# Kernel optimization log

Hardware: AMD Instinct MI355X
Metric: run time of the kernel (lower is better)

Reference implementation:

```python
import jax, jax.numpy as jnp
import numpy as np
from jax import lax

STEP_SIZE = 0.1
T0, T1 = 0.0, 1.0
NUM_STEPS = int(abs(T1 - T0) / STEP_SIZE)  # 10 leapfrog steps

B = 65536
N_DIM = 128      # q and p each have N_DIM dims; x has 2*N_DIM
HIDDEN = 512


def setup_inputs() -> dict:
    key = jax.random.key(0)
    k_x, k_w1, k_w2 = jax.random.split(key, 3)
    x = jax.random.normal(k_x, (B, 2 * N_DIM), dtype=jnp.float32)
    # potential MLP: Linear(N_DIM, HIDDEN) -> tanh -> Linear(HIDDEN, 1)
    W1 = jax.random.normal(k_w1, (N_DIM, HIDDEN), dtype=jnp.float32) / np.sqrt(N_DIM)
    b1 = jnp.zeros((HIDDEN,), dtype=jnp.float32)
    W2 = jax.random.normal(k_w2, (HIDDEN, 1), dtype=jnp.float32) / np.sqrt(HIDDEN)
    b2 = jnp.zeros((1,), dtype=jnp.float32)
    return {"x": x, "W1": W1, "b1": b1, "W2": W2, "b2": b2}


def reference(x, W1, b1, W2, b2):
    """Symplectic (leapfrog-style) forward integration of the Hamiltonian ODE.

    H(q,p) = 0.5*sum(p^2) + V(q), V(q) = MLP(q) with scalar output.
    Per step (faithful to the torch loop, grads taken jointly at (q,p)):
        dH/dq = dV/dq,  dH/dp = p
        p <- p - dV/dq * dt
        q <- q + p_old * dt
    """
    dt = jnp.float32(STEP_SIZE)
    n = x.shape[-1] // 2
    q0, p0 = x[..., :n], x[..., n:]

    def V_sum(q):  # sum over batch of scalar potential
        h = jnp.tanh(q @ W1 + b1)          # [B, HIDDEN]
        v = (h @ W2)[..., 0] + b2[0]       # [B]
        return v.sum()

    grad_V = jax.grad(V_sum)  # [B, n] -> dV/dq per sample (sum decouples)

    def step(carry, _):
        q, p = carry
        dH_dq = grad_V(q)      # grads at (q, p_old)
        dH_dp = p
        p_new = p - dH_dq * dt
        q_new = q + dH_dp * dt
        return (q_new, p_new), None

    (qf, pf), _ = lax.scan(step, (q0, p0), None, length=NUM_STEPS)
    return jnp.concatenate([qf, pf], axis=-1)
```

## Files before the change

### kernel.cpp

```cpp
#include <hip/hip_runtime.h>
#include <hip/hip_bf16.h>

typedef float f32x4 __attribute__((ext_vector_type(4)));
typedef __bf16 bf16x8 __attribute__((ext_vector_type(8)));
typedef unsigned short u16x4 __attribute__((ext_vector_type(4)));

#if defined(__has_builtin)
#if __has_builtin(__builtin_amdgcn_exp2f)
#define EXP2F(x) __builtin_amdgcn_exp2f(x)
#else
#define EXP2F(x) exp2f(x)
#endif
#if __has_builtin(__builtin_amdgcn_rcpf)
#define RCPF(x) __builtin_amdgcn_rcpf(x)
#else
#define RCPF(x) (1.0f/(x))
#endif
#else
#define EXP2F(x) exp2f(x)
#define RCPF(x) (1.0f/(x))
#endif

#define MFMA16(a,b,c) __builtin_amdgcn_mfma_f32_16x16x32_bf16((a),(b),(c),0,0,0)

__device__ __forceinline__ unsigned short f2bf(float f) {
  return __builtin_bit_cast(unsigned short, (__bf16)f);
}

__global__ __launch_bounds__(256) void hn_prep(const float* __restrict__ W1,
                                               unsigned short* __restrict__ W1T) {
  int t = blockIdx.x * 256 + threadIdx.x;
  int rho = t >> 7, io = t & 127;
  int j = (rho >> 5) * 32 + ((rho >> 2) & 3) * 8 + ((rho >> 4) & 1) * 4 + (rho & 3);
  int i = (io >> 5) * 32 + ((io & 7) >> 2) * 16 + ((io >> 3) & 3) * 4 + (io & 7 & 3);
  W1T[t] = f2bf(W1[i * 512 + j]);
}

__global__ __launch_bounds__(512, 2) void hn_main(
    const float* __restrict__ x, const float* __restrict__ W1,
    const float* __restrict__ b1, const float* __restrict__ W2,
    const unsigned short* __restrict__ W1T, float* __restrict__ out) {
  __shared__ __align__(16) char w1l[131072];
  __shared__ __align__(16) float b1s[512];
  __shared__ __align__(16) float w2s[512];

  const int tid = threadIdx.x;
  const int lane = tid & 63;
  const int w = tid >> 6;
  const int m = lane & 15;
  const int g = lane >> 4;

  for (int it = tid; it < 16384; it += 512) {
    int flat = it << 2;
    int i = flat >> 9;
    f32x4 v = *(const f32x4*)(W1 + flat);
    u16x4 pk;
#pragma unroll
    for (int c = 0; c < 4; ++c) pk[c] = f2bf(v[c]);
    int ba = flat << 1;
    *(u16x4*)(w1l + (ba ^ ((i & 7) << 4))) = pk;
  }
  if (tid < 512) {
    b1s[tid] = b1[tid] * 2.8853900817779268f;
    w2s[tid] = W2[tid];
  }
  __syncthreads();

  const int b0 = blockIdx.x * 256 + w * 32;

  float q[2][4][8], p[2][4][8];
#pragma unroll
  for (int bf = 0; bf < 2; ++bf)
#pragma unroll
    for (int kb = 0; kb < 4; ++kb) {
      const float* r0 = x + (long)(b0 + 16 * bf + m) * 256 + kb * 32 + g * 4;
#pragma unroll
      for (int h = 0; h < 2; ++h) {
        f32x4 qv = *(const f32x4*)(r0 + h * 16);
        f32x4 pv = *(const f32x4*)(r0 + h * 16 + 128);
#pragma unroll
        for (int rr = 0; rr < 4; ++rr) {
          q[bf][kb][4 * h + rr] = qv[rr];
          p[bf][kb][4 * h + rr] = pv[rr];
        }
      }
    }

  const char* aptr = (const char*)W1T + m * 256 + g * 16;
  const int s45 = (m & 3) << 4, s6 = (m & 4) << 4;
  const int ybase = ((m * 1024 + g * 16) ^ s45);

#pragma unroll 1
  for (int step = 0; step < 10; ++step) {
    f32x4 gacc[2][8];
#pragma unroll
    for (int bf = 0; bf < 2; ++bf)
#pragma unroll
      for (int nf = 0; nf < 8; ++nf) gacc[bf][nf] = f32x4{0.f, 0.f, 0.f, 0.f};

#pragma unroll 2
    for (int jblk = 0; jblk < 16; ++jblk) {
      f32x4 z[2][2];
      z[0][0] = f32x4{0.f,0.f,0.f,0.f}; z[0][1] = f32x4{0.f,0.f,0.f,0.f};
      z[1][0] = f32x4{0.f,0.f,0.f,0.f}; z[1][1] = f32x4{0.f,0.f,0.f,0.f};
#pragma unroll
      for (int kb = 0; kb < 4; ++kb) {
        bf16x8 qb0, qb1;
#pragma unroll
        for (int r = 0; r < 8; ++r) {
          qb0[r] = (__bf16)q[0][kb][r];
          qb1[r] = (__bf16)q[1][kb][r];
        }
#pragma unroll
        for (int jf = 0; jf < 2; ++jf) {
          bf16x8 a = *(const bf16x8*)(aptr + jblk * 8192 + jf * 4096 + kb * 64);
          z[jf][0] = MFMA16(a, qb0, z[jf][0]);
          z[jf][1] = MFMA16(a, qb1, z[jf][1]);
        }
      }
      float s8[2][8];
#pragma unroll
      for (int jf = 0; jf < 2; ++jf) {
        f32x4 b1v = *(const f32x4*)(b1s + jblk * 32 + g * 8 + jf * 4);
        f32x4 w2v = *(const f32x4*)(w2s + jblk * 32 + g * 8 + jf * 4);
#pragma unroll
        for (int bf = 0; bf < 2; ++bf)
#pragma unroll
          for (int rr = 0; rr < 4; ++rr) {
            float zz = fmaf(z[jf][bf][rr], 2.8853900817779268f, b1v[rr]);
            float e = EXP2F(zz);
            float u = RCPF(e + 1.f);
            float th = fmaf(-2.f, u, 1.f);
            s8[bf][jf * 4 + rr] = fmaf(-th * th, w2v[rr], w2v[rr]);
          }
      }
      bf16x8 sB0, sB1;
#pragma unroll
      for (int r = 0; r < 8; ++r) {
        sB0[r] = (__bf16)s8[0][r];
        sB1[r] = (__bf16)s8[1][r];
      }
      const int joff = (jblk * 64) ^ s6;
#pragma unroll
      for (int nf = 0; nf < 8; ++nf) {
        bf16x8 af = *(const bf16x8*)(w1l + ybase + nf * 16384 + joff);
        gacc[0][nf] = MFMA16(af, sB0, gacc[0][nf]);
        gacc[1][nf] = MFMA16(af, sB1, gacc[1][nf]);
      }
    }

#pragma unroll
    for (int bf = 0; bf < 2; ++bf)
#pragma unroll
      for (int kb = 0; kb < 4; ++kb)
#pragma unroll
        for (int r = 0; r < 8; ++r)
          q[bf][kb][r] = fmaf(0.1f, p[bf][kb][r], q[bf][kb][r]);

#pragma unroll
    for (int bf = 0; bf < 2; ++bf)
#pragma unroll
      for (int kb = 0; kb < 4; ++kb)
#pragma unroll
        for (int r = 0; r < 8; ++r)
          p[bf][kb][r] = fmaf(-0.1f, gacc[bf][2 * kb + (r >> 2)][r & 3], p[bf][kb][r]);

    __syncthreads();
  }

#pragma unroll
  for (int bf = 0; bf < 2; ++bf)
#pragma unroll
    for (int kb = 0; kb < 4; ++kb) {
      float* o = out + (long)(b0 + 16 * bf + m) * 256 + kb * 32 + g * 4;
#pragma unroll
      for (int h = 0; h < 2; ++h) {
        f32x4 qv, pv;
#pragma unroll
        for (int rr = 0; rr < 4; ++rr) {
          qv[rr] = q[bf][kb][4 * h + rr];
          pv[rr] = p[bf][kb][4 * h + rr];
        }
        *(f32x4*)(o + h * 16) = qv;
        *(f32x4*)(o + h * 16 + 128) = pv;
      }
    }
}

extern "C" void kernel_launch(void* const* d_in, const int* in_sizes, int n_in,
                              void* d_out, int out_size, void* d_ws, size_t ws_size,
                              hipStream_t stream) {
  const float* x  = (const float*)d_in[0];
  const float* W1 = (const float*)d_in[1];
  const float* b1 = (const float*)d_in[2];
  const float* W2 = (const float*)d_in[3];
  float* out = (float*)d_out;
  unsigned short* w1t = (unsigned short*)d_ws;

  hipLaunchKernelGGL(hn_prep, dim3(256), dim3(256), 0, stream, W1, w1t);
  hipLaunchKernelGGL(hn_main, dim3(256), dim3(512), 0, stream,
                     x, W1, b1, W2, w1t, out);
}
```

Measured before the change: 345.0 us.

## Use 1024-thread blocks with 16 rows per wave instead of 32

Each wave now handles one 16-row batch fragment instead of two, and each block has 16 waves of 1024 threads, so a block still covers 256 rows. The per-wave register footprint for q, p and the gradient accumulators is halved, which allows more waves per CU to hide MFMA and LDS latency. In exchange, every A-operand load from W1T and the LDS W1 fragments now feeds only one MFMA instead of two, which doubles load traffic per unit of compute. The 128KB LDS per block still limits residency, so the occupancy gain depends on how many blocks fit on a CU.

```diff
diff --git a/kernel.cpp b/kernel.cpp
--- a/kernel.cpp
+++ b/kernel.cpp
@@ -36,7 +36,7 @@
   W1T[t] = f2bf(W1[i * 512 + j]);
 }
 
-__global__ __launch_bounds__(512, 2) void hn_main(
+__global__ __launch_bounds__(1024, 4) void hn_main(
     const float* __restrict__ x, const float* __restrict__ W1,
     const float* __restrict__ b1, const float* __restrict__ W2,
     const unsigned short* __restrict__ W1T, float* __restrict__ out) {
@@ -50,7 +50,7 @@
   const int m = lane & 15;
   const int g = lane >> 4;
 
-  for (int it = tid; it < 16384; it += 512) {
+  for (int it = tid; it < 16384; it += 1024) {
     int flat = it << 2;
     int i = flat >> 9;
     f32x4 v = *(const f32x4*)(W1 + flat);
@@ -66,25 +66,24 @@
   }
   __syncthreads();
 
-  const int b0 = blockIdx.x * 256 + w * 32;
+  const int b0 = blockIdx.x * 256 + w * 16;
+  const float* xrow = x + (long)(b0 + m) * 256;
 
-  float q[2][4][8], p[2][4][8];
+  float q[4][8], p[4][8];
 #pragma unroll
-  for (int bf = 0; bf < 2; ++bf)
+  for (int kb = 0; kb < 4; ++kb) {
+    const float* r0 = xrow + kb * 32 + g * 4;
 #pragma unroll
-    for (int kb = 0; kb < 4; ++kb) {
-      const float* r0 = x + (long)(b0 + 16 * bf + m) * 256 + kb * 32 + g * 4;
+    for (int h = 0; h < 2; ++h) {
+      f32x4 qv = *(const f32x4*)(r0 + h * 16);
+      f32x4 pv = *(const f32x4*)(r0 + h * 16 + 128);
 #pragma unroll
-      for (int h = 0; h < 2; ++h) {
-        f32x4 qv = *(const f32x4*)(r0 + h * 16);
-        f32x4 pv = *(const f32x4*)(r0 + h * 16 + 128);
-#pragma unroll
-        for (int rr = 0; rr < 4; ++rr) {
-          q[bf][kb][4 * h + rr] = qv[rr];
-          p[bf][kb][4 * h + rr] = pv[rr];
-        }
+      for (int rr = 0; rr < 4; ++rr) {
+        q[kb][4 * h + rr] = qv[rr];
+        p[kb][4 * h + rr] = pv[rr];
       }
     }
+  }
 
   const char* aptr = (const char*)W1T + m * 256 + g * 16;
   const int s45 = (m & 3) << 4, s6 = (m & 4) << 4;
@@ -92,99 +91,79 @@
 
 #pragma unroll 1
   for (int step = 0; step < 10; ++step) {
-    f32x4 gacc[2][8];
+    f32x4 gacc[8];
 #pragma unroll
-    for (int bf = 0; bf < 2; ++bf)
-#pragma unroll
-      for (int nf = 0; nf < 8; ++nf) gacc[bf][nf] = f32x4{0.f, 0.f, 0.f, 0.f};
+    for (int nf = 0; nf < 8; ++nf) gacc[nf] = f32x4{0.f, 0.f, 0.f, 0.f};
 
 #pragma unroll 2
     for (int jblk = 0; jblk < 16; ++jblk) {
-      f32x4 z[2][2];
-      z[0][0] = f32x4{0.f,0.f,0.f,0.f}; z[0][1] = f32x4{0.f,0.f,0.f,0.f};
-      z[1][0] = f32x4{0.f,0.f,0.f,0.f}; z[1][1] = f32x4{0.f,0.f,0.f,0.f};
+      f32x4 z[2];
+      z[0] = f32x4{0.f, 0.f, 0.f, 0.f};
+      z[1] = f32x4{0.f, 0.f, 0.f, 0.f};
 #pragma unroll
       for (int kb = 0; kb < 4; ++kb) {
-        bf16x8 qb0, qb1;
+        bf16x8 qb;
 #pragma unroll
-        for (int r = 0; r < 8; ++r) {
-          qb0[r] = (__bf16)q[0][kb][r];
-          qb1[r] = (__bf16)q[1][kb][r];
-        }
+        for (int r = 0; r < 8; ++r) qb[r] = (__bf16)q[kb][r];
 #pragma unroll
         for (int jf = 0; jf < 2; ++jf) {
           bf16x8 a = *(const bf16x8*)(aptr + jblk * 8192 + jf * 4096 + kb * 64);
-          z[jf][0] = MFMA16(a, qb0, z[jf][0]);
-          z[jf][1] = MFMA16(a, qb1, z[jf][1]);
+          z[jf] = MFMA16(a, qb, z[jf]);
         }
       }
-      float s8[2][8];
+      bf16x8 sB;
 #pragma unroll
       for (int jf = 0; jf < 2; ++jf) {
         f32x4 b1v = *(const f32x4*)(b1s + jblk * 32 + g * 8 + jf * 4);
         f32x4 w2v = *(const f32x4*)(w2s + jblk * 32 + g * 8 + jf * 4);
 #pragma unroll
-        for (int bf = 0; bf < 2; ++bf)
-#pragma unroll
-          for (int rr = 0; rr < 4; ++rr) {
-            float zz = fmaf(z[jf][bf][rr], 2.8853900817779268f, b1v[rr]);
-            float e = EXP2F(zz);
-            float u = RCPF(e + 1.f);
-            float th = fmaf(-2.f, u, 1.f);
-            s8[bf][jf * 4 + rr] = fmaf(-th * th, w2v[rr], w2v[rr]);
-          }
-      }
-      bf16x8 sB0, sB1;
-#pragma unroll
-      for (int r = 0; r < 8; ++r) {
-        sB0[r] = (__bf16)s8[0][r];
-        sB1[r] = (__bf16)s8[1][r];
+        for (int rr = 0; rr < 4; ++rr) {
+          float zz = fmaf(z[jf][rr], 2.8853900817779268f, b1v[rr]);
+          float e = EXP2F(zz);
+          float u = RCPF(e + 1.f);
+          float th = fmaf(-2.f, u, 1.f);
+          sB[jf * 4 + rr] = (__bf16)fmaf(-th * th, w2v[rr], w2v[rr]);
+        }
       }
       const int joff = (jblk * 64) ^ s6;
 #pragma unroll
       for (int nf = 0; nf < 8; ++nf) {
         bf16x8 af = *(const bf16x8*)(w1l + ybase + nf * 16384 + joff);
-        gacc[0][nf] = MFMA16(af, sB0, gacc[0][nf]);
-        gacc[1][nf] = MFMA16(af, sB1, gacc[1][nf]);
+        gacc[nf] = MFMA16(af, sB, gacc[nf]);
       }
     }
 
 #pragma unroll
-    for (int bf = 0; bf < 2; ++bf)
+    for (int kb = 0; kb < 4; ++kb)
 #pragma unroll
-      for (int kb = 0; kb < 4; ++kb)
-#pragma unroll
-        for (int r = 0; r < 8; ++r)
-          q[bf][kb][r] = fmaf(0.1f, p[bf][kb][r], q[bf][kb][r]);
+      for (int r = 0; r < 8; ++r)
+        q[kb][r] = fmaf(0.1f, p[kb][r], q[kb][r]);
 
 #pragma unroll
-    for (int bf = 0; bf < 2; ++bf)
+    for (int kb = 0; kb < 4; ++kb)
 #pragma unroll
-      for (int kb = 0; kb < 4; ++kb)
-#pragma unroll
-        for (int r = 0; r < 8; ++r)
-          p[bf][kb][r] = fmaf(-0.1f, gacc[bf][2 * kb + (r >> 2)][r & 3], p[bf][kb][r]);
+      for (int r = 0; r < 8; ++r)
+        p[kb][r] = fmaf(-0.1f, gacc[2 * kb + (r >> 2)][r & 3], p[kb][r]);
 
     __syncthreads();
   }
 
+  float* orow = out + (long)(b0 + m) * 256;
 #pragma unroll
-  for (int bf = 0; bf < 2; ++bf)
+  for (int kb = 0; kb < 4; ++kb) {
+    float* o = orow + kb * 32 + g * 4;
 #pragma unroll
-    for (int kb = 0; kb < 4; ++kb) {
-      float* o = out + (long)(b0 + 16 * bf + m) * 256 + kb * 32 + g * 4;
+    for (int h = 0; h < 2; ++h) {
+      f32x4 qv, pv;
 #pragma unroll
-      for (int h = 0; h < 2; ++h) {
-        f32x4 qv, pv;
-#pragma unroll
-        for (int rr = 0; rr < 4; ++rr) {
-          qv[rr] = q[bf][kb][4 * h + rr];
-          pv[rr] = p[bf][kb][4 * h + rr];
-        }
-        *(f32x4*)(o + h * 16) = qv;
-        *(f32x4*)(o + h * 16 + 128) = pv;
+      for (int rr = 0; rr < 4; ++rr) {
+        qv[rr] = q[kb][4 * h + rr];
+        pv[rr] = p[kb][4 * h + rr];
       }
+      *(f32x4*)(o + h * 16) = qv;
+      *(f32x4*)(o + h * 16 + 128) = pv;
     }
+  }
 }
 
 extern "C" void kernel_launch(void* const* d_in, const int* in_sizes, int n_in,
@@ -198,6 +177,6 @@
   unsigned short* w1t = (unsigned short*)d_ws;
 
   hipLaunchKernelGGL(hn_prep, dim3(256), dim3(256), 0, stream, W1, w1t);
-  hipLaunchKernelGGL(hn_main, dim3(256), dim3(512), 0, stream,
+  hipLaunchKernelGGL(hn_main, dim3(256), dim3(1024), 0, stream,
                      x, W1, b1, W2, w1t, out);
 }
```

New measurement: 611.3 us. +77.2%, slower.

## Swap W1 operand placement: forward tile in LDS, backward from global bf16

Applied to the files above, without the earlier changes.

The prep kernel now writes both a permuted bf16 W1 for the forward matmul and a plain bf16 copy for the backward matmul. The main kernel stages the forward operand in LDS with an XOR swizzle and reads the backward operand straight from global/L2. This replaces per-block fp32-to-bf16 conversion with a plain copy. It also packs q and the tanh-derivative values with v_cvt_pk_bf16_f32 inline asm, hoists the q conversion out of the jblk loop, and drops the per-step __syncthreads. The cost is more global traffic in the backward loop (8 fragment loads per jblk now come from L2 instead of LDS), which may raise memory latency.

```diff
diff --git a/kernel.cpp b/kernel.cpp
--- a/kernel.cpp
+++ b/kernel.cpp
@@ -3,7 +3,8 @@
 
 typedef float f32x4 __attribute__((ext_vector_type(4)));
 typedef __bf16 bf16x8 __attribute__((ext_vector_type(8)));
-typedef unsigned short u16x4 __attribute__((ext_vector_type(4)));
+typedef unsigned int u32;
+typedef unsigned int u32x4 __attribute__((ext_vector_type(4)));
 
 #if defined(__has_builtin)
 #if __has_builtin(__builtin_amdgcn_exp2f)
@@ -27,20 +28,27 @@
   return __builtin_bit_cast(unsigned short, (__bf16)f);
 }
 
+__device__ __forceinline__ u32 pkbf(float a, float b) {
+  u32 d;
+  asm("v_cvt_pk_bf16_f32 %0, %1, %2" : "=v"(d) : "v"(a), "v"(b));
+  return d;
+}
+
 __global__ __launch_bounds__(256) void hn_prep(const float* __restrict__ W1,
-                                               unsigned short* __restrict__ W1T) {
+                                               unsigned short* __restrict__ ws) {
   int t = blockIdx.x * 256 + threadIdx.x;
   int rho = t >> 7, io = t & 127;
   int j = (rho >> 5) * 32 + ((rho >> 2) & 3) * 8 + ((rho >> 4) & 1) * 4 + (rho & 3);
-  int i = (io >> 5) * 32 + ((io & 7) >> 2) * 16 + ((io >> 3) & 3) * 4 + (io & 7 & 3);
-  W1T[t] = f2bf(W1[i * 512 + j]);
+  int i = (io >> 5) * 32 + ((io >> 2) & 1) * 16 + ((io >> 3) & 3) * 4 + (io & 3);
+  ws[t] = f2bf(W1[i * 512 + j]);
+  ws[65536 + t] = f2bf(W1[t]);
 }
 
 __global__ __launch_bounds__(512, 2) void hn_main(
     const float* __restrict__ x, const float* __restrict__ W1,
     const float* __restrict__ b1, const float* __restrict__ W2,
-    const unsigned short* __restrict__ W1T, float* __restrict__ out) {
-  __shared__ __align__(16) char w1l[131072];
+    const unsigned short* __restrict__ wsp, float* __restrict__ out) {
+  __shared__ __align__(16) char w1f[131072];
   __shared__ __align__(16) float b1s[512];
   __shared__ __align__(16) float w2s[512];
 
@@ -50,15 +58,12 @@
   const int m = lane & 15;
   const int g = lane >> 4;
 
-  for (int it = tid; it < 16384; it += 512) {
-    int flat = it << 2;
-    int i = flat >> 9;
-    f32x4 v = *(const f32x4*)(W1 + flat);
-    u16x4 pk;
-#pragma unroll
-    for (int c = 0; c < 4; ++c) pk[c] = f2bf(v[c]);
+  for (int it = tid; it < 8192; it += 512) {
+    int flat = it << 3;
+    int rho = flat >> 7;
+    u32x4 v = *(const u32x4*)(wsp + flat);
     int ba = flat << 1;
-    *(u16x4*)(w1l + (ba ^ ((i & 7) << 4))) = pk;
+    *(u32x4*)(w1f + (ba ^ ((rho & 7) << 4))) = v;
   }
   if (tid < 512) {
     b1s[tid] = b1[tid] * 2.8853900817779268f;
@@ -86,12 +91,26 @@
       }
     }
 
-  const char* aptr = (const char*)W1T + m * 256 + g * 16;
-  const int s45 = (m & 3) << 4, s6 = (m & 4) << 4;
-  const int ybase = ((m * 1024 + g * 16) ^ s45);
+  const int sw = (m & 7) << 4;
+  const int lbF[4] = {
+      (m * 256 + 0 * 64 + g * 16) ^ sw,
+      (m * 256 + 1 * 64 + g * 16) ^ sw,
+      (m * 256 + 2 * 64 + g * 16) ^ sw,
+      (m * 256 + 3 * 64 + g * 16) ^ sw};
+  const unsigned short* W1b = wsp + 65536;
+  const char* bptr = (const char*)W1b + m * 1024 + g * 16;
 
 #pragma unroll 1
   for (int step = 0; step < 10; ++step) {
+    u32x4 qbw[2][4];
+#pragma unroll
+    for (int bf = 0; bf < 2; ++bf)
+#pragma unroll
+      for (int kb = 0; kb < 4; ++kb)
+#pragma unroll
+        for (int h = 0; h < 4; ++h)
+          qbw[bf][kb][h] = pkbf(q[bf][kb][2 * h], q[bf][kb][2 * h + 1]);
+
     f32x4 gacc[2][8];
 #pragma unroll
     for (int bf = 0; bf < 2; ++bf)
@@ -105,45 +124,43 @@
       z[1][0] = f32x4{0.f,0.f,0.f,0.f}; z[1][1] = f32x4{0.f,0.f,0.f,0.f};
 #pragma unroll
       for (int kb = 0; kb < 4; ++kb) {
-        bf16x8 qb0, qb1;
-#pragma unroll
-        for (int r = 0; r < 8; ++r) {
-          qb0[r] = (__bf16)q[0][kb][r];
-          qb1[r] = (__bf16)q[1][kb][r];
-        }
-#pragma unroll
-        for (int jf = 0; jf < 2; ++jf) {
-          bf16x8 a = *(const bf16x8*)(aptr + jblk * 8192 + jf * 4096 + kb * 64);
-          z[jf][0] = MFMA16(a, qb0, z[jf][0]);
-          z[jf][1] = MFMA16(a, qb1, z[jf][1]);
-        }
-      }
-      float s8[2][8];
+        bf16x8 qb0 = __builtin_bit_cast(bf16x8, qbw[0][kb]);
+        bf16x8 qb1 = __builtin_bit_cast(bf16x8, qbw[1][kb]);
+        bf16x8 a0 = *(const bf16x8*)(w1f + lbF[kb] + jblk * 8192);
+        bf16x8 a1 = *(const bf16x8*)(w1f + lbF[kb] + jblk * 8192 + 4096);
+        z[0][0] = MFMA16(a0, qb0, z[0][0]);
+        z[0][1] = MFMA16(a0, qb1, z[0][1]);
+        z[1][0] = MFMA16(a1, qb0, z[1][0]);
+        z[1][1] = MFMA16(a1, qb1, z[1][1]);
+      }
+      u32x4 sp0, sp1;
 #pragma unroll
       for (int jf = 0; jf < 2; ++jf) {
         f32x4 b1v = *(const f32x4*)(b1s + jblk * 32 + g * 8 + jf * 4);
         f32x4 w2v = *(const f32x4*)(w2s + jblk * 32 + g * 8 + jf * 4);
 #pragma unroll
-        for (int bf = 0; bf < 2; ++bf)
+        for (int bf = 0; bf < 2; ++bf) {
+          const f32x4 zv = z[jf][bf];
+          float sv[4];
 #pragma unroll
           for (int rr = 0; rr < 4; ++rr) {
-            float zz = fmaf(z[jf][bf][rr], 2.8853900817779268f, b1v[rr]);
+            float zz = fmaf(zv[rr], 2.8853900817779268f, b1v[rr]);
             float e = EXP2F(zz);
             float u = RCPF(e + 1.f);
             float th = fmaf(-2.f, u, 1.f);
-            s8[bf][jf * 4 + rr] = fmaf(-th * th, w2v[rr], w2v[rr]);
+            sv[rr] = fmaf(-th * th, w2v[rr], w2v[rr]);
           }
-      }
-      bf16x8 sB0, sB1;
-#pragma unroll
-      for (int r = 0; r < 8; ++r) {
-        sB0[r] = (__bf16)s8[0][r];
-        sB1[r] = (__bf16)s8[1][r];
-      }
-      const int joff = (jblk * 64) ^ s6;
+          u32 w0 = pkbf(sv[0], sv[1]);
+          u32 w1p = pkbf(sv[2], sv[3]);
+          if (bf == 0) { sp0[jf * 2] = w0; sp0[jf * 2 + 1] = w1p; }
+          else         { sp1[jf * 2] = w0; sp1[jf * 2 + 1] = w1p; }
+        }
+      }
+      bf16x8 sB0 = __builtin_bit_cast(bf16x8, sp0);
+      bf16x8 sB1 = __builtin_bit_cast(bf16x8, sp1);
 #pragma unroll
       for (int nf = 0; nf < 8; ++nf) {
-        bf16x8 af = *(const bf16x8*)(w1l + ybase + nf * 16384 + joff);
+        bf16x8 af = *(const bf16x8*)(bptr + nf * 16384 + jblk * 64);
         gacc[0][nf] = MFMA16(af, sB0, gacc[0][nf]);
         gacc[1][nf] = MFMA16(af, sB1, gacc[1][nf]);
       }
@@ -164,8 +181,6 @@
 #pragma unroll
         for (int r = 0; r < 8; ++r)
           p[bf][kb][r] = fmaf(-0.1f, gacc[bf][2 * kb + (r >> 2)][r & 3], p[bf][kb][r]);
-
-    __syncthreads();
   }
 
 #pragma unroll
@@ -195,9 +210,9 @@
   const float* b1 = (const float*)d_in[2];
   const float* W2 = (const float*)d_in[3];
   float* out = (float*)d_out;
-  unsigned short* w1t = (unsigned short*)d_ws;
-
-  hipLaunchKernelGGL(hn_prep, dim3(256), dim3(256), 0, stream, W1, w1t);
+  unsigned short* wsp = (unsigned short*)d_ws;
+
+  hipLaunchKernelGGL(hn_prep, dim3(256), dim3(256), 0, stream, W1, wsp);
   hipLaunchKernelGGL(hn_main, dim3(256), dim3(512), 0, stream,
-                     x, W1, b1, W2, w1t, out);
-}
+                     x, W1, b1, W2, wsp, out);
+}
```

Result: no change. 351.4 us (+1.9%).
